# Kernel optimization log

Measured on AMD Instinct MI355X. Metric: run time of the kernel, lower is better.

## Reference

```python
import jax, jax.numpy as jnp
import numpy as np

B = 32768
D_A, D_V, D_T = 512, 512, 768
D_KW, D_CTX, D_SPK = 256, 256, 128
H = 512
IN_A = D_V + D_T + D_KW + D_CTX + D_SPK  # 1920 = visual + other_dim (text+hidden+speaker)
IN_V = D_A + D_T + D_KW + D_CTX + D_SPK  # 1920


def _linear_params(key, din, dout):
    kw, kb = jax.random.split(key)
    bound = 1.0 / np.sqrt(din)
    W = jax.random.uniform(kw, (din, dout), jnp.float32, -bound, bound)
    b = jax.random.uniform(kb, (dout,), jnp.float32, -bound, bound)
    return W, b


def setup_inputs() -> dict:
    key = jax.random.key(0)
    ks = jax.random.split(key, 16)
    inp = {
        'audio': jax.random.normal(ks[0], (B, D_A), jnp.float32),
        'visual': jax.random.normal(ks[1], (B, D_V), jnp.float32),
        'text': jax.random.normal(ks[2], (B, D_T), jnp.float32),
        'keywords': jax.random.normal(ks[3], (B, D_KW), jnp.float32),
        'context': jax.random.normal(ks[4], (B, D_CTX), jnp.float32),
        'speaker_embed': jax.random.normal(ks[5], (B, D_SPK), jnp.float32),
    }
    # Masks restricted to dimensionally-consistent patterns: [0,1,1] or [1,0,1]
    r = jax.random.randint(ks[6], (B,), 0, 2)
    inp['modality_masks'] = jnp.stack([r, 1 - r, jnp.ones_like(r)], axis=1).astype(jnp.int32)
    # audio_imagination MLP params
    inp['aW1'], inp['ab1'] = _linear_params(ks[7], IN_A, H)
    inp['aW2'], inp['ab2'] = _linear_params(ks[8], H, H)
    inp['aW3'], inp['ab3'] = _linear_params(ks[9], H, D_A)
    # visual_imagination MLP params
    inp['vW1'], inp['vb1'] = _linear_params(ks[10], IN_V, H)
    inp['vW2'], inp['vb2'] = _linear_params(ks[11], H, H)
    inp['vW3'], inp['vb3'] = _linear_params(ks[12], H, D_V)
    return inp


def _mlp(x, W1, b1, W2, b2, W3, b3):
    h = jax.nn.relu(x @ W1 + b1)  # dropout is eval-mode identity
    h = jax.nn.relu(h @ W2 + b2)
    return h @ W3 + b3


def reference(audio, visual, text, keywords, context, speaker_embed, modality_masks,
              aW1, ab1, aW2, ab2, aW3, ab3,
              vW1, vb1, vW2, vb2, vW3, vb3):
    m = modality_masks.astype(audio.dtype)
    common = jnp.concatenate([keywords, context, speaker_embed], axis=-1)  # [B, 640]
    in_a = jnp.concatenate([visual, text, common], axis=-1)  # [B, IN_A]
    in_v = jnp.concatenate([audio, text, common], axis=-1)   # [B, IN_V]
    # Rows where the modality is present (mask==1) were omitted in the original
    # ragged stacking; here they are zeroed to keep a fixed [B, D] output.
    recon_audio = _mlp(in_a, aW1, ab1, aW2, ab2, aW3, ab3) * (1.0 - m[:, 0:1])
    recon_visual = _mlp(in_v, vW1, vb1, vW2, vb2, vW3, vb3) * (1.0 - m[:, 1:2])
    return recon_audio, recon_visual
```

## Files before the change

kernel.cpp:

```cpp
#include <hip/hip_runtime.h>
#include <stdint.h>

typedef __bf16 bf16;
typedef __bf16 bf16x8 __attribute__((ext_vector_type(8)));
typedef float  f32x4  __attribute__((ext_vector_type(4)));

#define NROWS 32768
#define HID   512

__global__ void prep_transpose(const float* __restrict__ W, bf16* __restrict__ WT,
                               int K, int N) {
  __shared__ float t[32][33];
  int k0 = blockIdx.x * 32, n0 = blockIdx.y * 32;
  int tx = threadIdx.x, ty = threadIdx.y;
#pragma unroll
  for (int p = 0; p < 4; ++p)
    t[ty + p * 8][tx] = W[(size_t)(k0 + ty + p * 8) * N + n0 + tx];
  __syncthreads();
#pragma unroll
  for (int p = 0; p < 4; ++p)
    WT[(size_t)(n0 + ty + p * 8) * K + k0 + tx] = (bf16)t[tx][ty + p * 8];
}

__global__ void compact_rows(const int* __restrict__ masks, int* __restrict__ counts,
                             int* __restrict__ idxA, int* __restrict__ idxV) {
  int i = blockIdx.x * 256 + threadIdx.x;
  int lane = threadIdx.x & 63;
  int r = masks[i * 3];
  unsigned long long voteA = __ballot(r == 0);
  int nA = __popcll(voteA);
  int baseA = 0, baseV = 0;
  if (lane == 0) {
    baseA = atomicAdd(&counts[0], nA);
    baseV = atomicAdd(&counts[1], 64 - nA);
  }
  baseA = __shfl(baseA, 0);
  baseV = __shfl(baseV, 0);
  unsigned long long ltmask = (lane == 63) ? ~0ULL >> 1 : (1ULL << lane) - 1;
  int posA = __popcll(voteA & ltmask);
  int posV = lane - posA;
  if (r == 0) idxA[baseA + posA] = i;
  else        idxV[baseV + posV] = i;
}

template <int LAYER>
__global__ __launch_bounds__(256) void mlp_gemm(
    const float* __restrict__ audio, const float* __restrict__ visual,
    const float* __restrict__ text,  const float* __restrict__ kwd,
    const float* __restrict__ ctx,   const float* __restrict__ spk,
    const bf16*  __restrict__ hin,
    const bf16*  __restrict__ WTa,   const bf16* __restrict__ WTv,
    const float* __restrict__ ba,    const float* __restrict__ bv,
    const int*   __restrict__ counts,
    const int*   __restrict__ idxA,  const int* __restrict__ idxV,
    bf16* __restrict__ hout, float* __restrict__ out) {
  constexpr int K = (LAYER == 1) ? 1920 : 512;
  const int mlp = blockIdx.z;
  const int cnt = counts[mlp];
  const int m0 = blockIdx.x * 128;
  if (m0 >= cnt) return;
  const int n0 = blockIdx.y * 128;
  const bf16*  WT   = mlp ? WTv : WTa;
  const float* bias = mlp ? bv : ba;
  const int*   idx  = mlp ? idxV : idxA;

  __shared__ __attribute__((aligned(16))) bf16 sA[128 * 64];
  __shared__ __attribute__((aligned(16))) bf16 sB[128 * 64];

  const int t = threadIdx.x;
  const int lane = t & 63;
  const int wave = t >> 6;
  const int wm = (wave >> 1) * 64;
  const int wn = (wave & 1) * 64;

  int gidx[4];
  if constexpr (LAYER == 1) {
#pragma unroll
    for (int rep = 0; rep < 4; ++rep) {
      int row = (t + rep * 256) >> 3;
      int i = m0 + row;
      if (i >= cnt) i = cnt - 1;
      gidx[rep] = idx[i];
    }
  }

  const f32x4 fzero = {0.f, 0.f, 0.f, 0.f};
  f32x4 acc[4][4];
#pragma unroll
  for (int a = 0; a < 4; ++a)
#pragma unroll
    for (int b = 0; b < 4; ++b) acc[a][b] = fzero;

  for (int k0 = 0; k0 < K; k0 += 64) {
    const float* seg = nullptr;
    int soff = 0, sstr = 0;
    if constexpr (LAYER == 1) {
      if (k0 < 512)       { seg = mlp ? audio : visual; soff = k0;        sstr = 512; }
      else if (k0 < 1280) { seg = text; soff = k0 - 512;  sstr = 768; }
      else if (k0 < 1536) { seg = kwd;  soff = k0 - 1280; sstr = 256; }
      else if (k0 < 1792) { seg = ctx;  soff = k0 - 1536; sstr = 256; }
      else                { seg = spk;  soff = k0 - 1792; sstr = 128; }
    }
    __syncthreads();
#pragma unroll
    for (int rep = 0; rep < 4; ++rep) {
      int slot = t + rep * 256;
      int row = slot >> 3, c = slot & 7;
      int wc = c ^ (row & 7);
      bf16x8 v;
      if constexpr (LAYER == 1) {
        const float* src = seg + (size_t)gidx[rep] * sstr + soff + c * 8;
        f32x4 lo = *(const f32x4*)src;
        f32x4 hi = *(const f32x4*)(src + 4);
        v[0] = (bf16)lo[0]; v[1] = (bf16)lo[1]; v[2] = (bf16)lo[2]; v[3] = (bf16)lo[3];
        v[4] = (bf16)hi[0]; v[5] = (bf16)hi[1]; v[6] = (bf16)hi[2]; v[7] = (bf16)hi[3];
      } else {
        const bf16* src = hin + ((size_t)mlp * NROWS + m0 + row) * HID + k0 + c * 8;
        v = *(const bf16x8*)src;
      }
      *(bf16x8*)&sA[row * 64 + wc * 8] = v;
      const bf16* bsrc = WT + (size_t)(n0 + row) * K + k0 + c * 8;
      *(bf16x8*)&sB[row * 64 + wc * 8] = *(const bf16x8*)bsrc;
    }
    __syncthreads();

    bf16x8 af[4][2], bfr[4][2];
#pragma unroll
    for (int mf = 0; mf < 4; ++mf)
#pragma unroll
      for (int kh = 0; kh < 2; ++kh) {
        int row = wm + mf * 16 + (lane & 15);
        int c = (lane >> 4) + kh * 4;
        af[mf][kh] = *(const bf16x8*)&sA[row * 64 + (c ^ (row & 7)) * 8];
      }
#pragma unroll
    for (int nf = 0; nf < 4; ++nf)
#pragma unroll
      for (int kh = 0; kh < 2; ++kh) {
        int row = wn + nf * 16 + (lane & 15);
        int c = (lane >> 4) + kh * 4;
        bfr[nf][kh] = *(const bf16x8*)&sB[row * 64 + (c ^ (row & 7)) * 8];
      }
#pragma unroll
    for (int mf = 0; mf < 4; ++mf)
#pragma unroll
      for (int nf = 0; nf < 4; ++nf)
#pragma unroll
        for (int kh = 0; kh < 2; ++kh)
          acc[mf][nf] = __builtin_amdgcn_mfma_f32_16x16x32_bf16(
              af[mf][kh], bfr[nf][kh], acc[mf][nf], 0, 0, 0);
  }

  const int r4 = (lane >> 4) * 4;
  const int cl = lane & 15;
#pragma unroll
  for (int mf = 0; mf < 4; ++mf) {
#pragma unroll
    for (int reg = 0; reg < 4; ++reg) {
      int lrow = wm + mf * 16 + r4 + reg;
      int grow = m0 + lrow;
      if (grow >= cnt) continue;
      if constexpr (LAYER < 3) {
#pragma unroll
        for (int nf = 0; nf < 4; ++nf) {
          int col = n0 + wn + nf * 16 + cl;
          float v = acc[mf][nf][reg] + bias[col];
          v = fmaxf(v, 0.f);
          hout[((size_t)mlp * NROWS + grow) * HID + col] = (bf16)v;
        }
      } else {
        int g = idx[grow];
#pragma unroll
        for (int nf = 0; nf < 4; ++nf) {
          int col = n0 + wn + nf * 16 + cl;
          float v = acc[mf][nf][reg] + bias[col];
          out[((size_t)mlp * NROWS + g) * 512 + col] = v;
          out[((size_t)(1 - mlp) * NROWS + g) * 512 + col] = 0.f;
        }
      }
    }
  }
}

extern "C" void kernel_launch(void* const* d_in, const int* in_sizes, int n_in,
                              void* d_out, int out_size, void* d_ws, size_t ws_size,
                              hipStream_t stream) {
  (void)in_sizes; (void)n_in; (void)out_size;
  const float* audio  = (const float*)d_in[0];
  const float* visual = (const float*)d_in[1];
  const float* text   = (const float*)d_in[2];
  const float* kwd    = (const float*)d_in[3];
  const float* ctx    = (const float*)d_in[4];
  const float* spk    = (const float*)d_in[5];
  const int*   masks  = (const int*)d_in[6];
  const float* aW1 = (const float*)d_in[7];  const float* ab1 = (const float*)d_in[8];
  const float* aW2 = (const float*)d_in[9];  const float* ab2 = (const float*)d_in[10];
  const float* aW3 = (const float*)d_in[11]; const float* ab3 = (const float*)d_in[12];
  const float* vW1 = (const float*)d_in[13]; const float* vb1 = (const float*)d_in[14];
  const float* vW2 = (const float*)d_in[15]; const float* vb2 = (const float*)d_in[16];
  const float* vW3 = (const float*)d_in[17]; const float* vb3 = (const float*)d_in[18];
  float* out = (float*)d_out;

  char* w = (char*)d_ws;
  int* counts = (int*)w;
  int* idxA = (int*)(w + 4096);
  int* idxV = idxA + 32768;
  bf16* aW1t = (bf16*)(w + 4096 + 262144);
  bf16* vW1t = aW1t + 983040;
  bf16* aW2t = vW1t + 983040;
  bf16* vW2t = aW2t + 262144;
  bf16* aW3t = vW2t + 262144;
  bf16* vW3t = aW3t + 262144;
  bf16* h1 = vW3t + 262144;
  bf16* h2 = h1 + (size_t)2 * NROWS * HID;
  (void)ws_size;

  hipMemsetAsync(counts, 0, 8, stream);
  dim3 tb(32, 8);
  prep_transpose<<<dim3(60, 16), tb, 0, stream>>>(aW1, aW1t, 1920, 512);
  prep_transpose<<<dim3(60, 16), tb, 0, stream>>>(vW1, vW1t, 1920, 512);
  prep_transpose<<<dim3(16, 16), tb, 0, stream>>>(aW2, aW2t, 512, 512);
  prep_transpose<<<dim3(16, 16), tb, 0, stream>>>(vW2, vW2t, 512, 512);
  prep_transpose<<<dim3(16, 16), tb, 0, stream>>>(aW3, aW3t, 512, 512);
  prep_transpose<<<dim3(16, 16), tb, 0, stream>>>(vW3, vW3t, 512, 512);
  compact_rows<<<128, 256, 0, stream>>>(masks, counts, idxA, idxV);

  dim3 gg(256, 4, 2);
  mlp_gemm<1><<<gg, 256, 0, stream>>>(audio, visual, text, kwd, ctx, spk, nullptr,
                                      aW1t, vW1t, ab1, vb1, counts, idxA, idxV, h1, nullptr);
  mlp_gemm<2><<<gg, 256, 0, stream>>>(audio, visual, text, kwd, ctx, spk, h1,
                                      aW2t, vW2t, ab2, vb2, counts, idxA, idxV, h2, nullptr);
  mlp_gemm<3><<<gg, 256, 0, stream>>>(audio, visual, text, kwd, ctx, spk, h2,
                                      aW3t, vW3t, ab3, vb3, counts, idxA, idxV, nullptr, out);
}
```

Measured before the change: 264.0 us.

## Double-buffer GEMM tiles with direct global-to-LDS loads and pre-swizzled layouts

The K-loop now uses two LDS buffers so the loads for the next tile are issued before the MFMAs on the current tile run. Weights and intermediate activations are pre-swizzled in global memory, which lets them go straight into LDS through global_load_lds without a register round-trip. Layer-1 activations are still gathered into registers, converted to bf16 and written to LDS after compute, and occupancy is hinted with launch_bounds(256,2). Doubling the LDS footprint and the added register pressure may limit occupancy.

```diff
diff --git a/kernel.cpp b/kernel.cpp
--- a/kernel.cpp
+++ b/kernel.cpp
@@ -7,6 +7,12 @@
 
 #define NROWS 32768
 #define HID   512
+
+__device__ __forceinline__ void gload_lds16(const void* g, void* l) {
+  __builtin_amdgcn_global_load_lds(
+      (const __attribute__((address_space(1))) void*)g,
+      (__attribute__((address_space(3))) void*)l, 16, 0, 0);
+}
 
 __global__ void prep_transpose(const float* __restrict__ W, bf16* __restrict__ WT,
                                int K, int N) {
@@ -18,8 +24,12 @@
     t[ty + p * 8][tx] = W[(size_t)(k0 + ty + p * 8) * N + n0 + tx];
   __syncthreads();
 #pragma unroll
-  for (int p = 0; p < 4; ++p)
-    WT[(size_t)(n0 + ty + p * 8) * K + k0 + tx] = (bf16)t[tx][ty + p * 8];
+  for (int p = 0; p < 4; ++p) {
+    int n = n0 + ty + p * 8;
+    int k = k0 + tx;
+    int ks = (k & ~63) | (((((k >> 3) & 7) ^ (n & 7))) << 3) | (k & 7);
+    WT[(size_t)n * K + ks] = (bf16)t[tx][ty + p * 8];
+  }
 }
 
 __global__ void compact_rows(const int* __restrict__ masks, int* __restrict__ counts,
@@ -44,7 +54,7 @@
 }
 
 template <int LAYER>
-__global__ __launch_bounds__(256) void mlp_gemm(
+__global__ __launch_bounds__(256, 2) void mlp_gemm(
     const float* __restrict__ audio, const float* __restrict__ visual,
     const float* __restrict__ text,  const float* __restrict__ kwd,
     const float* __restrict__ ctx,   const float* __restrict__ spk,
@@ -55,6 +65,7 @@
     const int*   __restrict__ idxA,  const int* __restrict__ idxV,
     bf16* __restrict__ hout, float* __restrict__ out) {
   constexpr int K = (LAYER == 1) ? 1920 : 512;
+  constexpr int NT = K / 64;
   const int mlp = blockIdx.z;
   const int cnt = counts[mlp];
   const int m0 = blockIdx.x * 128;
@@ -64,8 +75,8 @@
   const float* bias = mlp ? bv : ba;
   const int*   idx  = mlp ? idxV : idxA;
 
-  __shared__ __attribute__((aligned(16))) bf16 sA[128 * 64];
-  __shared__ __attribute__((aligned(16))) bf16 sB[128 * 64];
+  __shared__ __attribute__((aligned(16))) bf16 sA[2][128 * 64];
+  __shared__ __attribute__((aligned(16))) bf16 sB[2][128 * 64];
 
   const int t = threadIdx.x;
   const int lane = t & 63;
@@ -84,46 +95,79 @@
     }
   }
 
-  const f32x4 fzero = {0.f, 0.f, 0.f, 0.f};
-  f32x4 acc[4][4];
-#pragma unroll
-  for (int a = 0; a < 4; ++a)
-#pragma unroll
-    for (int b = 0; b < 4; ++b) acc[a][b] = fzero;
-
-  for (int k0 = 0; k0 < K; k0 += 64) {
-    const float* seg = nullptr;
-    int soff = 0, sstr = 0;
-    if constexpr (LAYER == 1) {
-      if (k0 < 512)       { seg = mlp ? audio : visual; soff = k0;        sstr = 512; }
-      else if (k0 < 1280) { seg = text; soff = k0 - 512;  sstr = 768; }
-      else if (k0 < 1536) { seg = kwd;  soff = k0 - 1280; sstr = 256; }
-      else if (k0 < 1792) { seg = ctx;  soff = k0 - 1536; sstr = 256; }
-      else                { seg = spk;  soff = k0 - 1792; sstr = 128; }
-    }
-    __syncthreads();
+  f32x4 pa[4], pb[4];
+
+  auto B_ISSUE = [&](int k0, int buf) {
+#pragma unroll
+    for (int j = 0; j < 4; ++j) {
+      int sbase = (wave * 4 + j) * 64;
+      int slot = sbase + lane;
+      int row = slot >> 3, wc = slot & 7;
+      gload_lds16(WT + (size_t)(n0 + row) * K + k0 + wc * 8, &sB[buf][sbase * 8]);
+    }
+  };
+  auto A_ISSUE_LDS = [&](int k0, int buf) {
+#pragma unroll
+    for (int j = 0; j < 4; ++j) {
+      int sbase = (wave * 4 + j) * 64;
+      int slot = sbase + lane;
+      int row = slot >> 3, wc = slot & 7;
+      gload_lds16(hin + ((size_t)mlp * NROWS + m0 + row) * HID + k0 + wc * 8,
+                  &sA[buf][sbase * 8]);
+    }
+  };
+  auto A_ISSUE = [&](int k0) {
+    const float* seg; int soff, sstr;
+    if (k0 < 512)       { seg = mlp ? audio : visual; soff = k0;        sstr = 512; }
+    else if (k0 < 1280) { seg = text; soff = k0 - 512;  sstr = 768; }
+    else if (k0 < 1536) { seg = kwd;  soff = k0 - 1280; sstr = 256; }
+    else if (k0 < 1792) { seg = ctx;  soff = k0 - 1536; sstr = 256; }
+    else                { seg = spk;  soff = k0 - 1792; sstr = 128; }
+#pragma unroll
+    for (int rep = 0; rep < 4; ++rep) {
+      int slot = t + rep * 256;
+      int c = slot & 7;
+      const float* src = seg + (size_t)gidx[rep] * sstr + soff + c * 8;
+      pa[rep] = *(const f32x4*)src;
+      pb[rep] = *(const f32x4*)(src + 4);
+    }
+  };
+  auto A_WRITE = [&](int buf) {
 #pragma unroll
     for (int rep = 0; rep < 4; ++rep) {
       int slot = t + rep * 256;
       int row = slot >> 3, c = slot & 7;
       int wc = c ^ (row & 7);
       bf16x8 v;
-      if constexpr (LAYER == 1) {
-        const float* src = seg + (size_t)gidx[rep] * sstr + soff + c * 8;
-        f32x4 lo = *(const f32x4*)src;
-        f32x4 hi = *(const f32x4*)(src + 4);
-        v[0] = (bf16)lo[0]; v[1] = (bf16)lo[1]; v[2] = (bf16)lo[2]; v[3] = (bf16)lo[3];
-        v[4] = (bf16)hi[0]; v[5] = (bf16)hi[1]; v[6] = (bf16)hi[2]; v[7] = (bf16)hi[3];
-      } else {
-        const bf16* src = hin + ((size_t)mlp * NROWS + m0 + row) * HID + k0 + c * 8;
-        v = *(const bf16x8*)src;
-      }
-      *(bf16x8*)&sA[row * 64 + wc * 8] = v;
-      const bf16* bsrc = WT + (size_t)(n0 + row) * K + k0 + c * 8;
-      *(bf16x8*)&sB[row * 64 + wc * 8] = *(const bf16x8*)bsrc;
-    }
-    __syncthreads();
-
+      v[0] = (bf16)pa[rep][0]; v[1] = (bf16)pa[rep][1];
+      v[2] = (bf16)pa[rep][2]; v[3] = (bf16)pa[rep][3];
+      v[4] = (bf16)pb[rep][0]; v[5] = (bf16)pb[rep][1];
+      v[6] = (bf16)pb[rep][2]; v[7] = (bf16)pb[rep][3];
+      *(bf16x8*)&sA[buf][row * 64 + wc * 8] = v;
+    }
+  };
+
+  const f32x4 fzero = {0.f, 0.f, 0.f, 0.f};
+  f32x4 acc[4][4];
+#pragma unroll
+  for (int a = 0; a < 4; ++a)
+#pragma unroll
+    for (int b = 0; b < 4; ++b) acc[a][b] = fzero;
+
+  if constexpr (LAYER == 1) { A_ISSUE(0); A_WRITE(0); }
+  else                      { A_ISSUE_LDS(0, 0); }
+  B_ISSUE(0, 0);
+  __syncthreads();
+
+  int cur = 0;
+  for (int ti = 0; ti < NT; ++ti) {
+    const int k0 = ti * 64;
+    const bool pf = (ti + 1 < NT);
+    if (pf) {
+      if constexpr (LAYER == 1) A_ISSUE(k0 + 64);
+      else                      A_ISSUE_LDS(k0 + 64, cur ^ 1);
+      B_ISSUE(k0 + 64, cur ^ 1);
+    }
     bf16x8 af[4][2], bfr[4][2];
 #pragma unroll
     for (int mf = 0; mf < 4; ++mf)
@@ -131,7 +175,7 @@
       for (int kh = 0; kh < 2; ++kh) {
         int row = wm + mf * 16 + (lane & 15);
         int c = (lane >> 4) + kh * 4;
-        af[mf][kh] = *(const bf16x8*)&sA[row * 64 + (c ^ (row & 7)) * 8];
+        af[mf][kh] = *(const bf16x8*)&sA[cur][row * 64 + (c ^ (row & 7)) * 8];
       }
 #pragma unroll
     for (int nf = 0; nf < 4; ++nf)
@@ -139,7 +183,7 @@
       for (int kh = 0; kh < 2; ++kh) {
         int row = wn + nf * 16 + (lane & 15);
         int c = (lane >> 4) + kh * 4;
-        bfr[nf][kh] = *(const bf16x8*)&sB[row * 64 + (c ^ (row & 7)) * 8];
+        bfr[nf][kh] = *(const bf16x8*)&sB[cur][row * 64 + (c ^ (row & 7)) * 8];
       }
 #pragma unroll
     for (int mf = 0; mf < 4; ++mf)
@@ -149,6 +193,11 @@
         for (int kh = 0; kh < 2; ++kh)
           acc[mf][nf] = __builtin_amdgcn_mfma_f32_16x16x32_bf16(
               af[mf][kh], bfr[nf][kh], acc[mf][nf], 0, 0, 0);
+    if constexpr (LAYER == 1) {
+      if (pf) A_WRITE(cur ^ 1);
+    }
+    __syncthreads();
+    cur ^= 1;
   }
 
   const int r4 = (lane >> 4) * 4;
@@ -166,7 +215,8 @@
           int col = n0 + wn + nf * 16 + cl;
           float v = acc[mf][nf][reg] + bias[col];
           v = fmaxf(v, 0.f);
-          hout[((size_t)mlp * NROWS + grow) * HID + col] = (bf16)v;
+          int cs = (col & ~63) | (((((col >> 3) & 7) ^ (grow & 7))) << 3) | (col & 7);
+          hout[((size_t)mlp * NROWS + grow) * HID + cs] = (bf16)v;
         }
       } else {
         int g = idx[grow];
```

Measured after the change: 290.7 us. 10.1% more time.
